# Kernel optimization log

Measured on AMD Instinct MI355X. Metric: run time of the kernel, lower is better.

The kernel has to match this reference:

```python
import jax, jax.numpy as jnp
import numpy as np

B, T, D_IN = 256, 250, 700
H1, H2, D_OUT = 256, 256, 20
B_J0 = 0.01
BETA = 1.8  # adaptation strength (isAdapt=1)
LENS, SCALE, HIGHT, GAMMA = 0.5, 6.0, 0.15, 0.5
SQRT_2PI = float(np.sqrt(2.0 * np.pi))


def _gaussian(x, mu, sigma):
    return jnp.exp(-((x - mu) ** 2) / (2.0 * sigma ** 2)) / (SQRT_2PI * sigma)


@jax.custom_vjp
def act_fun(x):
    # Heaviside spike with multi-Gaussian surrogate gradient (gradient_type='MG')
    return (x > 0).astype(x.dtype)


def _act_fwd(x):
    return act_fun(x), x


def _act_bwd(x, g):
    temp = (_gaussian(x, 0.0, LENS) * (1.0 + HIGHT)
            - _gaussian(x, LENS, SCALE * LENS) * HIGHT
            - _gaussian(x, -LENS, SCALE * LENS) * HIGHT)
    return (g * temp * GAMMA,)


act_fun.defvjp(_act_fwd, _act_bwd)


def setup_inputs() -> dict:
    key = jax.random.key(0)
    ks = jax.random.split(key, 16)
    # binary-ish spike input (SHD spike trains), rand fill
    x = (jax.random.uniform(ks[0], (B, T, D_IN)) < 0.1).astype(jnp.float32)

    def xavier(k, out_d, in_d):
        lim = float(np.sqrt(6.0 / (in_d + out_d)))
        return jax.random.uniform(k, (out_d, in_d), jnp.float32, -lim, lim)

    return {
        "x": x,
        "w_i2h1": xavier(ks[1], H1, D_IN),
        "w_h12h1": xavier(ks[2], H1, H1),
        "w_h12h2": xavier(ks[3], H2, H1),
        "w_h22h2": xavier(ks[4], H2, H2),
        "w_h2o": xavier(ks[5], D_OUT, H2),
        "b_h1": jnp.zeros((H1,), jnp.float32),
        "b_h2": jnp.zeros((H2,), jnp.float32),
        "b_o": jnp.zeros((D_OUT,), jnp.float32),
        "tau_adp_h1": 150.0 + 10.0 * jax.random.normal(ks[6], (H1,), jnp.float32),
        "tau_adp_h2": 150.0 + 10.0 * jax.random.normal(ks[7], (H2,), jnp.float32),
        "tau_m_h1": 20.0 + 5.0 * jax.random.normal(ks[8], (H1,), jnp.float32),
        "tau_m_h2": 20.0 + 5.0 * jax.random.normal(ks[9], (H2,), jnp.float32),
        "tau_m_o": 20.0 + 5.0 * jax.random.normal(ks[10], (D_OUT,), jnp.float32),
    }


def _lif_step(inp, mem, spk, b, alpha, ro):
    # mem_update_adp with params=None, dparams=None, isAdapt=1, dt=1, R_m=1
    b = ro * b + BETA * (1.0 - ro) * spk
    mem = mem * alpha - b * spk + (1.0 - alpha) * inp
    spk = act_fun(mem - b - B_J0)
    return mem, spk, b


def reference(x, w_i2h1, w_h12h1, w_h12h2, w_h22h2, w_h2o,
              b_h1, b_h2, b_o, tau_adp_h1, tau_adp_h2,
              tau_m_h1, tau_m_h2, tau_m_o):
    bsz = x.shape[0]
    h1, h2, d_out = w_i2h1.shape[0], w_h12h2.shape[0], w_h2o.shape[0]

    alpha1 = jnp.exp(-1.0 / tau_m_h1)
    ro1 = jnp.exp(-1.0 / tau_adp_h1)
    alpha2 = jnp.exp(-1.0 / tau_m_h2)
    ro2 = jnp.exp(-1.0 / tau_adp_h2)
    alpha_o = jnp.exp(-1.0 / tau_m_o)

    init = (
        jnp.zeros((bsz, h1)), jnp.zeros((bsz, h1)), jnp.full((bsz, h1), B_J0),
        jnp.zeros((bsz, h2)), jnp.zeros((bsz, h2)), jnp.full((bsz, h2), B_J0),
        jnp.zeros((bsz, d_out)), jnp.zeros((bsz, d_out)),
    )
    xT = jnp.swapaxes(x, 0, 1)  # [T, B, D_in]

    def step(carry, xt):
        mem1, spk1, bb1, mem2, spk2, bb2, mem_o, acc = carry
        h1_in = xt @ w_i2h1.T + spk1 @ w_h12h1.T + b_h1
        mem1, spk1, bb1 = _lif_step(h1_in, mem1, spk1, bb1, alpha1, ro1)
        h2_in = spk1 @ w_h12h2.T + spk2 @ w_h22h2.T + b_h2
        mem2, spk2, bb2 = _lif_step(h2_in, mem2, spk2, bb2, alpha2, ro2)
        o_in = spk2 @ w_h2o.T + b_o
        mem_o = mem_o * alpha_o + (1.0 - alpha_o) * o_in  # output_Neuron
        acc = acc + jax.nn.softmax(mem_o, axis=-1)
        return (mem1, spk1, bb1, mem2, spk2, bb2, mem_o, acc), None

    carry, _ = jax.lax.scan(step, init, xT)
    return carry[-1]  # accumulated softmax over the 250 timesteps, [B, 20]
```

## Files before the change

kernel.cpp:

```cpp
#include <hip/hip_runtime.h>
#include <cstdint>
#include <cstddef>

#define BB 256
#define TT 250
#define DIN 700
#define H1 256
#define H2 256
#define DOUT 20
#define BJ0 0.01f
#define BETAC 1.8f
#define IQSCALE 3.814697265625e-06f

typedef float f32x4 __attribute__((ext_vector_type(4)));
typedef short s16x4 __attribute__((ext_vector_type(4)));
typedef int   i32x4 __attribute__((ext_vector_type(4)));

#define COFF_BL  180224
#define SOFF_T11 180224
#define SOFF_T12 245760
#define SOFF_T22 311296
#define FOFF_W2O 188416
#define FOFF_XP  193536
#define FOFF_MO  16577536
#define N_TRANS  381952

#define BARRIER_LDS() asm volatile("s_waitcnt lgkmcnt(0)\n\ts_barrier" ::: "memory")

__device__ __forceinline__ short q18(float w) {
    float s = w * 262144.0f;
    s = fminf(fmaxf(s, -32767.0f), 32767.0f);
    return (short)__float2int_rn(s);
}

__global__ void transpose_all_k(const float* __restrict__ w_i2h1,
                                const float* __restrict__ w_h12h1,
                                const float* __restrict__ w_h12h2,
                                const float* __restrict__ w_h22h2,
                                const float* __restrict__ w_h2o,
                                signed char* __restrict__ cws,
                                short* __restrict__ sws,
                                float* __restrict__ fws) {
    int i = blockIdx.x * blockDim.x + threadIdx.x;
    if (i < 180224) {
        int h = i / 704, k = i - h * 704;
        int q = (k < DIN) ? (int)q18(w_i2h1[h * DIN + k]) : 0;
        q = q > 32639 ? 32639 : (q < -32640 ? -32640 : q);
        int hi = (q + 128) >> 8;
        int lo = q - (hi << 8);
        cws[i] = (signed char)hi;
        cws[COFF_BL + i] = (signed char)lo;
        return;
    }
    i -= 180224;
    if (i < 65536) { int d = i >> 8, h = i & 255;
        sws[SOFF_T11 + i] = q18(w_h12h1[h * H1 + d]); return; }
    i -= 65536;
    if (i < 65536) { int d = i >> 8, h = i & 255;
        sws[SOFF_T12 + i] = q18(w_h12h2[h * H1 + d]); return; }
    i -= 65536;
    if (i < 65536) { int d = i >> 8, h = i & 255;
        sws[SOFF_T22 + i] = q18(w_h22h2[h * H2 + d]); return; }
    i -= 65536;
    if (i < 5120)  { int j = i / 20, o = i % 20;
        fws[FOFF_W2O + i] = w_h2o[o * H2 + j]; return; }
}

__global__ __launch_bounds__(256) void xgemm_k(const float* __restrict__ x,
                                               const signed char* __restrict__ Bh,
                                               const signed char* __restrict__ Bl,
                                               const float* __restrict__ b_h1,
                                               float* __restrict__ Xp) {
    const int t    = threadIdx.x;
    const int lane = t & 63;
    const int w    = t >> 6;
    const int m0   = blockIdx.x * 32;

    __shared__ __align__(16) signed char Asub[32 * 720];
    __shared__ __align__(16) signed char Bhs[256 * 80];
    __shared__ __align__(16) signed char Bls[256 * 80];

    #pragma unroll
    for (int it = 0; it < 22; ++it) {
        int flat = it * 256 + t;
        int row  = flat / 176;
        int c4   = flat - row * 176;
        unsigned int pk = 0u;
        if (c4 < 175) {
            const float* xr = x + (size_t)(m0 + row) * DIN;
            float4 f = *(const float4*)(xr + (c4 << 2));
            pk = (f.x != 0.f ? 1u : 0u)
               | (f.y != 0.f ? 1u : 0u) << 8
               | (f.z != 0.f ? 1u : 0u) << 16
               | (f.w != 0.f ? 1u : 0u) << 24;
        }
        *(unsigned int*)(Asub + row * 720 + (c4 << 2)) = pk;
    }

    i32x4 acch[2][4], accl[2][4];
    #pragma unroll
    for (int mt = 0; mt < 2; ++mt)
        #pragma unroll
        for (int nt = 0; nt < 4; ++nt) {
            acch[mt][nt] = (i32x4){0, 0, 0, 0};
            accl[mt][nt] = (i32x4){0, 0, 0, 0};
        }

    const int arow  = lane & 15;
    const int kg16  = (lane >> 4) << 4;
    const int bcol0 = w << 6;

    for (int ks = 0; ks < 11; ++ks) {
        __syncthreads();
        #pragma unroll
        for (int it2 = 0; it2 < 4; ++it2) {
            int row = it2 * 64 + (t >> 2);
            int ch  = (t & 3) << 4;
            int go  = row * 704 + ks * 64 + ch;
            *(int4*)(Bhs + row * 80 + ch) = *(const int4*)(Bh + go);
            *(int4*)(Bls + row * 80 + ch) = *(const int4*)(Bl + go);
        }
        __syncthreads();

        const int ko = ks * 64 + kg16;
        i32x4 a0 = *(const i32x4*)(Asub + arow * 720 + ko);
        i32x4 a1 = *(const i32x4*)(Asub + (16 + arow) * 720 + ko);
        #pragma unroll
        for (int nt = 0; nt < 4; ++nt) {
            const int bb = (bcol0 + nt * 16 + arow) * 80 + kg16;
            i32x4 bhf = *(const i32x4*)(Bhs + bb);
            i32x4 blf = *(const i32x4*)(Bls + bb);
            acch[0][nt] = __builtin_amdgcn_mfma_i32_16x16x64_i8(a0, bhf, acch[0][nt], 0, 0, 0);
            acch[1][nt] = __builtin_amdgcn_mfma_i32_16x16x64_i8(a1, bhf, acch[1][nt], 0, 0, 0);
            accl[0][nt] = __builtin_amdgcn_mfma_i32_16x16x64_i8(a0, blf, accl[0][nt], 0, 0, 0);
            accl[1][nt] = __builtin_amdgcn_mfma_i32_16x16x64_i8(a1, blf, accl[1][nt], 0, 0, 0);
        }
    }

    const int crb = (lane >> 4) << 2;
    #pragma unroll
    for (int nt = 0; nt < 4; ++nt) {
        int col = bcol0 + nt * 16 + arow;
        float bias = b_h1[col];
        #pragma unroll
        for (int mt = 0; mt < 2; ++mt) {
            #pragma unroll
            for (int r = 0; r < 4; ++r) {
                int row = m0 + mt * 16 + crb + r;
                int ir = (acch[mt][nt][r] << 8) + accl[mt][nt][r];
                __builtin_nontemporal_store(bias + (float)ir * IQSCALE,
                                            Xp + (size_t)row * H1 + col);
            }
        }
    }
}

__device__ __forceinline__ void add8v(const short* __restrict__ T,
                                      const int* __restrict__ L, int off,
                                      int* a) {
    int4 ea = *(const int4*)(L + off);
    int4 eb = *(const int4*)(L + off + 4);
    s16x4 w0 = *(const s16x4*)(T + ((size_t)ea.x << 8));
    s16x4 w1 = *(const s16x4*)(T + ((size_t)ea.y << 8));
    s16x4 w2 = *(const s16x4*)(T + ((size_t)ea.z << 8));
    s16x4 w3 = *(const s16x4*)(T + ((size_t)ea.w << 8));
    s16x4 w4 = *(const s16x4*)(T + ((size_t)eb.x << 8));
    s16x4 w5 = *(const s16x4*)(T + ((size_t)eb.y << 8));
    s16x4 w6 = *(const s16x4*)(T + ((size_t)eb.z << 8));
    s16x4 w7 = *(const s16x4*)(T + ((size_t)eb.w << 8));
    a[0] += ((w0.x + w1.x) + (w2.x + w3.x)) + ((w4.x + w5.x) + (w6.x + w7.x));
    a[1] += ((w0.y + w1.y) + (w2.y + w3.y)) + ((w4.y + w5.y) + (w6.y + w7.y));
    a[2] += ((w0.z + w1.z) + (w2.z + w3.z)) + ((w4.z + w5.z) + (w6.z + w7.z));
    a[3] += ((w0.w + w1.w) + (w2.w + w3.w)) + ((w4.w + w5.w) + (w6.w + w7.w));
}

__device__ __forceinline__ void tailv(const short* __restrict__ T,
                                      const int* __restrict__ L, int done,
                                      int rem, int* a) {
    if (rem >= 4) {
        int4 e = *(const int4*)(L + done);
        s16x4 w0 = *(const s16x4*)(T + ((size_t)e.x << 8));
        s16x4 w1 = *(const s16x4*)(T + ((size_t)e.y << 8));
        s16x4 w2 = *(const s16x4*)(T + ((size_t)e.z << 8));
        s16x4 w3 = *(const s16x4*)(T + ((size_t)e.w << 8));
        a[0] += (w0.x + w1.x) + (w2.x + w3.x);
        a[1] += (w0.y + w1.y) + (w2.y + w3.y);
        a[2] += (w0.z + w1.z) + (w2.z + w3.z);
        a[3] += (w0.w + w1.w) + (w2.w + w3.w);
        done += 4; rem -= 4;
    }
    if (rem) {
        int4 e = *(const int4*)(L + done);
        s16x4 w0 = *(const s16x4*)(T + ((size_t)e.x << 8));
        a[0] += w0.x; a[1] += w0.y; a[2] += w0.z; a[3] += w0.w;
        if (rem > 1) {
            s16x4 w1 = *(const s16x4*)(T + ((size_t)e.y << 8));
            a[0] += w1.x; a[1] += w1.y; a[2] += w1.z; a[3] += w1.w;
        }
        if (rem > 2) {
            s16x4 w2 = *(const s16x4*)(T + ((size_t)e.z << 8));
            a[0] += w2.x; a[1] += w2.y; a[2] += w2.z; a[3] += w2.w;
        }
    }
}

__device__ __forceinline__ void add8f(const float* __restrict__ T,
                                      const int* __restrict__ L, int off,
                                      float& acc) {
    int4 ea = *(const int4*)(L + off);
    int4 eb = *(const int4*)(L + off + 4);
    acc += T[ea.x * DOUT]; acc += T[ea.y * DOUT];
    acc += T[ea.z * DOUT]; acc += T[ea.w * DOUT];
    acc += T[eb.x * DOUT]; acc += T[eb.y * DOUT];
    acc += T[eb.z * DOUT]; acc += T[eb.w * DOUT];
}

__device__ __forceinline__ void tailf(const float* __restrict__ T,
                                      const int* __restrict__ L, int done,
                                      int rem, float& acc) {
    if (rem >= 4) {
        int4 e = *(const int4*)(L + done);
        acc += T[e.x * DOUT]; acc += T[e.y * DOUT];
        acc += T[e.z * DOUT]; acc += T[e.w * DOUT];
        done += 4; rem -= 4;
    }
    if (rem) {
        int4 e = *(const int4*)(L + done);
        acc += T[e.x * DOUT];
        if (rem > 1) acc += T[e.y * DOUT];
        if (rem > 2) acc += T[e.z * DOUT];
    }
}

__global__ __launch_bounds__(128) void rec_k(
    const float* __restrict__ Xp,
    const short* __restrict__ sT11, const short* __restrict__ sT12,
    const short* __restrict__ sT22, const float* __restrict__ wT2o,
    const float* __restrict__ b_h2, const float* __restrict__ b_o,
    const float* __restrict__ tau_adp_h1, const float* __restrict__ tau_adp_h2,
    const float* __restrict__ tau_m_h1, const float* __restrict__ tau_m_h2,
    const float* __restrict__ tau_m_o,
    float* __restrict__ Mo) {
    const int tid  = threadIdx.x;
    const int lane = tid & 63;
    const int w    = tid >> 6;
    const int c0   = lane << 2;
    const int b    = blockIdx.x;
    const float* __restrict__ XpB = Xp + (size_t)b * TT * H1;
    float* __restrict__ MoB = Mo + (size_t)b * TT * DOUT;

    __shared__ __align__(16) float w2oL[5120];
    __shared__ __align__(16) int lst1s[2][256];
    __shared__ __align__(16) int lst2s[2][256];
    __shared__ int lcnt[2][2];

    for (int k = tid; k < 5120; k += 128) w2oL[k] = wT2o[k];
    for (int k = tid; k < 256; k += 128) {
        lst1s[0][k] = 0; lst1s[1][k] = 0;
        lst2s[0][k] = 0; lst2s[1][k] = 0;
    }
    if (tid < 4) ((int*)lcnt)[tid] = 0;

    float alpha[4], rr[4], inb[4];
    #pragma unroll
    for (int s = 0; s < 4; ++s) {
        if (w == 0) {
            alpha[s] = expf(-1.0f / tau_m_h1[c0 + s]);
            rr[s]    = expf(-1.0f / tau_adp_h1[c0 + s]);
            inb[s]   = 0.f;
        } else {
            alpha[s] = expf(-1.0f / tau_m_h2[c0 + s]);
            rr[s]    = expf(-1.0f / tau_adp_h2[c0 + s]);
            inb[s]   = b_h2[c0 + s];
        }
    }
    float alpo = 0.f, bov = 0.f;
    if (w == 0 && lane < DOUT) { alpo = expf(-1.0f / tau_m_o[lane]); bov = b_o[lane]; }

    float mem[4] = {0.f, 0.f, 0.f, 0.f};
    float bb[4]  = {BJ0, BJ0, BJ0, BJ0};
    float spk[4] = {0.f, 0.f, 0.f, 0.f};
    float memo = 0.f;

    f32x4 xp_cur = (f32x4){0.f, 0.f, 0.f, 0.f};
    if (w == 0) xp_cur = *(const f32x4*)(XpB + c0);
    __syncthreads();

    for (int i = 0; i <= TT + 1; ++i) {
        const int cur = i & 1, nxt = cur ^ 1;

        const int tot1 = lcnt[cur][0];
        const int tot2 = lcnt[cur][1];

        f32x4 xp_nxt = (f32x4){0.f, 0.f, 0.f, 0.f};
        if (w == 0 && i + 1 < TT)
            xp_nxt = *(const f32x4*)(XpB + (size_t)(i + 1) * H1 + c0);

        const int* __restrict__ L1l = lst1s[cur];
        const int* __restrict__ L2l = lst2s[cur];

        int a1[4] = {0, 0, 0, 0};
        int a2[4] = {0, 0, 0, 0};
        float ao = 0.f;

        if (w == 0) {
            if (i < TT) {
                const short* colT = sT11 + c0;
                const int nb8 = tot1 >> 3;
                for (int kk = 0; kk < nb8; ++kk) add8v(colT, L1l, kk << 3, a1);
                tailv(colT, L1l, nb8 << 3, tot1 & 7, a1);
            }
            if (lane < DOUT && i >= 2) {
                const float* colO = w2oL + lane;
                const int nb8 = tot2 >> 3;
                for (int kk = 0; kk < nb8; ++kk) add8f(colO, L2l, kk << 3, ao);
                tailf(colO, L2l, nb8 << 3, tot2 & 7, ao);
            }
        } else if (i >= 1 && i <= TT) {
            const short* cT12 = sT12 + c0;
            const short* cT22 = sT22 + c0;
            const int nb81 = tot1 >> 3;
            const int nb82 = tot2 >> 3;
            const int nbm = nb81 > nb82 ? nb81 : nb82;
            for (int kk = 0; kk < nbm; ++kk) {
                if (kk < nb81) add8v(cT12, L1l, kk << 3, a1);
                if (kk < nb82) add8v(cT22, L2l, kk << 3, a2);
            }
            tailv(cT12, L1l, nb81 << 3, tot1 & 7, a1);
            tailv(cT22, L2l, nb82 << 3, tot2 & 7, a2);
        }

        if (w == 0) {
            int tot = 0;
            if (i < TT) {
                unsigned long long Ms[4];
                #pragma unroll
                for (int s = 0; s < 4; ++s) {
                    float r1 = (float)a1[s] * IQSCALE;
                    bb[s]  = rr[s] * bb[s] + BETAC * (1.f - rr[s]) * spk[s];
                    mem[s] = mem[s] * alpha[s] - bb[s] * spk[s]
                           + (1.f - alpha[s]) * (xp_cur[s] + r1);
                    float ns = (mem[s] - bb[s] - BJ0) > 0.f ? 1.f : 0.f;
                    spk[s] = ns;
                    Ms[s] = __ballot(ns != 0.f ? 1 : 0);
                }
                const unsigned long long below = (1ull << lane) - 1ull;
                int p0 = __popcll(Ms[0]), p1 = __popcll(Ms[1]);
                int p2 = __popcll(Ms[2]), p3 = __popcll(Ms[3]);
                int b1 = p0, b2 = p0 + p1, b3 = p0 + p1 + p2;
                tot = b3 + p3;
                if (spk[0] != 0.f) lst1s[nxt][__popcll(Ms[0] & below)]      = c0;
                if (spk[1] != 0.f) lst1s[nxt][b1 + __popcll(Ms[1] & below)] = c0 + 1;
                if (spk[2] != 0.f) lst1s[nxt][b2 + __popcll(Ms[2] & below)] = c0 + 2;
                if (spk[3] != 0.f) lst1s[nxt][b3 + __popcll(Ms[3] & below)] = c0 + 3;
            }
            if (lane == 0) lcnt[nxt][0] = tot;
            if (lane < DOUT && i >= 2) {
                memo = memo * alpo + (1.f - alpo) * (bov + ao);
                __builtin_nontemporal_store(memo, MoB + (size_t)(i - 2) * DOUT + lane);
            }
        } else {
            int tot = 0;
            if (i >= 1 && i <= TT) {
                unsigned long long Ms[4];
                #pragma unroll
                for (int s = 0; s < 4; ++s) {
                    float r23 = (float)(a1[s] + a2[s]) * IQSCALE;
                    bb[s]  = rr[s] * bb[s] + BETAC * (1.f - rr[s]) * spk[s];
                    mem[s] = mem[s] * alpha[s] - bb[s] * spk[s]
                           + (1.f - alpha[s]) * (inb[s] + r23);
                    float ns = (mem[s] - bb[s] - BJ0) > 0.f ? 1.f : 0.f;
                    spk[s] = ns;
                    Ms[s] = __ballot(ns != 0.f ? 1 : 0);
                }
                const unsigned long long below = (1ull << lane) - 1ull;
                int p0 = __popcll(Ms[0]), p1 = __popcll(Ms[1]);
                int p2 = __popcll(Ms[2]), p3 = __popcll(Ms[3]);
                int b1 = p0, b2 = p0 + p1, b3 = p0 + p1 + p2;
                tot = b3 + p3;
                if (spk[0] != 0.f) lst2s[nxt][__popcll(Ms[0] & below)]      = c0;
                if (spk[1] != 0.f) lst2s[nxt][b1 + __popcll(Ms[1] & below)] = c0 + 1;
                if (spk[2] != 0.f) lst2s[nxt][b2 + __popcll(Ms[2] & below)] = c0 + 2;
                if (spk[3] != 0.f) lst2s[nxt][b3 + __popcll(Ms[3] & below)] = c0 + 3;
            }
            if (lane == 0) lcnt[nxt][1] = tot;
        }

        BARRIER_LDS();
        xp_cur = xp_nxt;
    }
}

__global__ __launch_bounds__(256) void soft_k(const float* __restrict__ Mo,
                                              float* __restrict__ out) {
    const int b = blockIdx.x;
    const int t = threadIdx.x;
    __shared__ float sm[TT][DOUT];

    if (t < TT) {
        const float* row = Mo + ((size_t)b * TT + t) * DOUT;
        float v[DOUT];
        #pragma unroll
        for (int k = 0; k < DOUT; k += 4) {
            float4 r = *(const float4*)(row + k);
            v[k] = r.x; v[k + 1] = r.y; v[k + 2] = r.z; v[k + 3] = r.w;
        }
        float mx = v[0];
        #pragma unroll
        for (int j = 1; j < DOUT; ++j) mx = fmaxf(mx, v[j]);
        float s = 0.f;
        #pragma unroll
        for (int j = 0; j < DOUT; ++j) { v[j] = __expf(v[j] - mx); s += v[j]; }
        float inv = 1.0f / s;
        #pragma unroll
        for (int j = 0; j < DOUT; ++j) sm[t][j] = v[j] * inv;
    }
    __syncthreads();
    if (t < DOUT) {
        float acc = 0.f;
        for (int tt = 0; tt < TT; ++tt) acc += sm[tt][t];
        out[b * DOUT + t] = acc;
    }
}

extern "C" void kernel_launch(void* const* d_in, const int* in_sizes, int n_in,
                              void* d_out, int out_size, void* d_ws, size_t ws_size,
                              hipStream_t stream) {
    const float* x          = (const float*)d_in[0];
    const float* w_i2h1     = (const float*)d_in[1];
    const float* w_h12h1    = (const float*)d_in[2];
    const float* w_h12h2    = (const float*)d_in[3];
    const float* w_h22h2    = (const float*)d_in[4];
    const float* w_h2o      = (const float*)d_in[5];
    const float* b_h1       = (const float*)d_in[6];
    const float* b_h2       = (const float*)d_in[7];
    const float* b_o        = (const float*)d_in[8];
    const float* tau_adp_h1 = (const float*)d_in[9];
    const float* tau_adp_h2 = (const float*)d_in[10];
    const float* tau_m_h1   = (const float*)d_in[11];
    const float* tau_m_h2   = (const float*)d_in[12];
    const float* tau_m_o    = (const float*)d_in[13];

    signed char* cws = (signed char*)d_ws;
    short* sws = (short*)d_ws;
    float* fws = (float*)d_ws;
    const signed char* Bh = cws;
    const signed char* Bl = cws + COFF_BL;
    const short* sT11 = sws + SOFF_T11;
    const short* sT12 = sws + SOFF_T12;
    const short* sT22 = sws + SOFF_T22;
    float* wT2o = fws + FOFF_W2O;
    float* Xp   = fws + FOFF_XP;
    float* Mo   = fws + FOFF_MO;

    transpose_all_k<<<N_TRANS / 256, 256, 0, stream>>>(
        w_i2h1, w_h12h1, w_h12h2, w_h22h2, w_h2o, cws, sws, fws);

    xgemm_k<<<(BB * TT) / 32, 256, 0, stream>>>(x, Bh, Bl, b_h1, Xp);

    rec_k<<<BB, 128, 0, stream>>>(Xp, sT11, sT12, sT22, wT2o,
                                  b_h2, b_o, tau_adp_h1, tau_adp_h2,
                                  tau_m_h1, tau_m_h2, tau_m_o, Mo);

    soft_k<<<BB, 256, 0, stream>>>(Mo, (float*)d_out);
}
```

Measured before the change: 753.5 us.

## Merge two recurrent-layer waves into one wavefront to drop block barriers

```diff
diff --git a/kernel.cpp b/kernel.cpp
--- a/kernel.cpp
+++ b/kernel.cpp
@@ -24,8 +24,6 @@
 #define FOFF_XP  193536
 #define FOFF_MO  16577536
 #define N_TRANS  381952
-
-#define BARRIER_LDS() asm volatile("s_waitcnt lgkmcnt(0)\n\ts_barrier" ::: "memory")
 
 __device__ __forceinline__ short q18(float w) {
     float s = w * 262144.0f;
@@ -232,7 +230,7 @@
     }
 }
 
-__global__ __launch_bounds__(128) void rec_k(
+__global__ __launch_bounds__(64) void rec_k(
     const float* __restrict__ Xp,
     const short* __restrict__ sT11, const short* __restrict__ sT12,
     const short* __restrict__ sT22, const float* __restrict__ wT2o,
@@ -241,9 +239,7 @@
     const float* __restrict__ tau_m_h1, const float* __restrict__ tau_m_h2,
     const float* __restrict__ tau_m_o,
     float* __restrict__ Mo) {
-    const int tid  = threadIdx.x;
-    const int lane = tid & 63;
-    const int w    = tid >> 6;
+    const int lane = threadIdx.x;
     const int c0   = lane << 2;
     const int b    = blockIdx.x;
     const float* __restrict__ XpB = Xp + (size_t)b * TT * H1;
@@ -252,141 +248,134 @@
     __shared__ __align__(16) float w2oL[5120];
     __shared__ __align__(16) int lst1s[2][256];
     __shared__ __align__(16) int lst2s[2][256];
-    __shared__ int lcnt[2][2];
-
-    for (int k = tid; k < 5120; k += 128) w2oL[k] = wT2o[k];
-    for (int k = tid; k < 256; k += 128) {
+
+    for (int k = lane; k < 5120; k += 64) w2oL[k] = wT2o[k];
+    for (int k = lane; k < 256; k += 64) {
         lst1s[0][k] = 0; lst1s[1][k] = 0;
         lst2s[0][k] = 0; lst2s[1][k] = 0;
     }
-    if (tid < 4) ((int*)lcnt)[tid] = 0;
-
-    float alpha[4], rr[4], inb[4];
+
+    float a1c[4], r1c[4], a2c[4], r2c[4], inb[4];
     #pragma unroll
     for (int s = 0; s < 4; ++s) {
-        if (w == 0) {
-            alpha[s] = expf(-1.0f / tau_m_h1[c0 + s]);
-            rr[s]    = expf(-1.0f / tau_adp_h1[c0 + s]);
-            inb[s]   = 0.f;
-        } else {
-            alpha[s] = expf(-1.0f / tau_m_h2[c0 + s]);
-            rr[s]    = expf(-1.0f / tau_adp_h2[c0 + s]);
-            inb[s]   = b_h2[c0 + s];
-        }
+        a1c[s] = expf(-1.0f / tau_m_h1[c0 + s]);
+        r1c[s] = expf(-1.0f / tau_adp_h1[c0 + s]);
+        a2c[s] = expf(-1.0f / tau_m_h2[c0 + s]);
+        r2c[s] = expf(-1.0f / tau_adp_h2[c0 + s]);
+        inb[s] = b_h2[c0 + s];
     }
     float alpo = 0.f, bov = 0.f;
-    if (w == 0 && lane < DOUT) { alpo = expf(-1.0f / tau_m_o[lane]); bov = b_o[lane]; }
-
-    float mem[4] = {0.f, 0.f, 0.f, 0.f};
-    float bb[4]  = {BJ0, BJ0, BJ0, BJ0};
-    float spk[4] = {0.f, 0.f, 0.f, 0.f};
+    if (lane < DOUT) { alpo = expf(-1.0f / tau_m_o[lane]); bov = b_o[lane]; }
+
+    float mem1[4] = {0.f, 0.f, 0.f, 0.f};
+    float bb1[4]  = {BJ0, BJ0, BJ0, BJ0};
+    float spk1[4] = {0.f, 0.f, 0.f, 0.f};
+    float mem2[4] = {0.f, 0.f, 0.f, 0.f};
+    float bb2[4]  = {BJ0, BJ0, BJ0, BJ0};
+    float spk2[4] = {0.f, 0.f, 0.f, 0.f};
     float memo = 0.f;
-
-    f32x4 xp_cur = (f32x4){0.f, 0.f, 0.f, 0.f};
-    if (w == 0) xp_cur = *(const f32x4*)(XpB + c0);
+    int t1c = 0, t2c = 0;
+
+    f32x4 xp_cur = *(const f32x4*)(XpB + c0);
     __syncthreads();
 
     for (int i = 0; i <= TT + 1; ++i) {
         const int cur = i & 1, nxt = cur ^ 1;
 
-        const int tot1 = lcnt[cur][0];
-        const int tot2 = lcnt[cur][1];
-
         f32x4 xp_nxt = (f32x4){0.f, 0.f, 0.f, 0.f};
-        if (w == 0 && i + 1 < TT)
+        if (i + 1 < TT)
             xp_nxt = *(const f32x4*)(XpB + (size_t)(i + 1) * H1 + c0);
 
         const int* __restrict__ L1l = lst1s[cur];
         const int* __restrict__ L2l = lst2s[cur];
-
-        int a1[4] = {0, 0, 0, 0};
-        int a2[4] = {0, 0, 0, 0};
+        const bool d1 = (i < TT);
+        const bool d2 = (i >= 1 && i <= TT);
+        const int nb1 = t1c >> 3, rem1 = t1c & 7;
+        const int nb2 = t2c >> 3, rem2 = t2c & 7;
+
+        int A11[4] = {0, 0, 0, 0};
+        int A12[4] = {0, 0, 0, 0};
+        int A22[4] = {0, 0, 0, 0};
         float ao = 0.f;
 
-        if (w == 0) {
-            if (i < TT) {
-                const short* colT = sT11 + c0;
-                const int nb8 = tot1 >> 3;
-                for (int kk = 0; kk < nb8; ++kk) add8v(colT, L1l, kk << 3, a1);
-                tailv(colT, L1l, nb8 << 3, tot1 & 7, a1);
-            }
-            if (lane < DOUT && i >= 2) {
-                const float* colO = w2oL + lane;
-                const int nb8 = tot2 >> 3;
-                for (int kk = 0; kk < nb8; ++kk) add8f(colO, L2l, kk << 3, ao);
-                tailf(colO, L2l, nb8 << 3, tot2 & 7, ao);
-            }
-        } else if (i >= 1 && i <= TT) {
+        {
+            const short* cT11 = sT11 + c0;
             const short* cT12 = sT12 + c0;
             const short* cT22 = sT22 + c0;
-            const int nb81 = tot1 >> 3;
-            const int nb82 = tot2 >> 3;
-            const int nbm = nb81 > nb82 ? nb81 : nb82;
+            const int nbm = nb1 > nb2 ? nb1 : nb2;
             for (int kk = 0; kk < nbm; ++kk) {
-                if (kk < nb81) add8v(cT12, L1l, kk << 3, a1);
-                if (kk < nb82) add8v(cT22, L2l, kk << 3, a2);
+                if (d1 && kk < nb1) add8v(cT11, L1l, kk << 3, A11);
+                if (d2 && kk < nb1) add8v(cT12, L1l, kk << 3, A12);
+                if (d2 && kk < nb2) add8v(cT22, L2l, kk << 3, A22);
             }
-            tailv(cT12, L1l, nb81 << 3, tot1 & 7, a1);
-            tailv(cT22, L2l, nb82 << 3, tot2 & 7, a2);
-        }
-
-        if (w == 0) {
-            int tot = 0;
-            if (i < TT) {
-                unsigned long long Ms[4];
-                #pragma unroll
-                for (int s = 0; s < 4; ++s) {
-                    float r1 = (float)a1[s] * IQSCALE;
-                    bb[s]  = rr[s] * bb[s] + BETAC * (1.f - rr[s]) * spk[s];
-                    mem[s] = mem[s] * alpha[s] - bb[s] * spk[s]
-                           + (1.f - alpha[s]) * (xp_cur[s] + r1);
-                    float ns = (mem[s] - bb[s] - BJ0) > 0.f ? 1.f : 0.f;
-                    spk[s] = ns;
-                    Ms[s] = __ballot(ns != 0.f ? 1 : 0);
-                }
-                const unsigned long long below = (1ull << lane) - 1ull;
-                int p0 = __popcll(Ms[0]), p1 = __popcll(Ms[1]);
-                int p2 = __popcll(Ms[2]), p3 = __popcll(Ms[3]);
-                int b1 = p0, b2 = p0 + p1, b3 = p0 + p1 + p2;
-                tot = b3 + p3;
-                if (spk[0] != 0.f) lst1s[nxt][__popcll(Ms[0] & below)]      = c0;
-                if (spk[1] != 0.f) lst1s[nxt][b1 + __popcll(Ms[1] & below)] = c0 + 1;
-                if (spk[2] != 0.f) lst1s[nxt][b2 + __popcll(Ms[2] & below)] = c0 + 2;
-                if (spk[3] != 0.f) lst1s[nxt][b3 + __popcll(Ms[3] & below)] = c0 + 3;
+            if (d1) tailv(cT11, L1l, nb1 << 3, rem1, A11);
+            if (d2) {
+                tailv(cT12, L1l, nb1 << 3, rem1, A12);
+                tailv(cT22, L2l, nb2 << 3, rem2, A22);
             }
-            if (lane == 0) lcnt[nxt][0] = tot;
-            if (lane < DOUT && i >= 2) {
-                memo = memo * alpo + (1.f - alpo) * (bov + ao);
-                __builtin_nontemporal_store(memo, MoB + (size_t)(i - 2) * DOUT + lane);
+        }
+        if (lane < DOUT && i >= 2) {
+            const float* colO = w2oL + lane;
+            for (int kk = 0; kk < nb2; ++kk) add8f(colO, L2l, kk << 3, ao);
+            tailf(colO, L2l, nb2 << 3, rem2, ao);
+        }
+
+        const unsigned long long below = (1ull << lane) - 1ull;
+
+        if (d1) {
+            unsigned long long Ms[4];
+            #pragma unroll
+            for (int s = 0; s < 4; ++s) {
+                float r1 = (float)A11[s] * IQSCALE;
+                bb1[s]  = r1c[s] * bb1[s] + BETAC * (1.f - r1c[s]) * spk1[s];
+                mem1[s] = mem1[s] * a1c[s] - bb1[s] * spk1[s]
+                        + (1.f - a1c[s]) * (xp_cur[s] + r1);
+                float ns = (mem1[s] - bb1[s] - BJ0) > 0.f ? 1.f : 0.f;
+                spk1[s] = ns;
+                Ms[s] = __ballot(ns != 0.f ? 1 : 0);
             }
+            int p0 = __popcll(Ms[0]), p1 = __popcll(Ms[1]);
+            int p2 = __popcll(Ms[2]), p3 = __popcll(Ms[3]);
+            int o1 = p0, o2 = p0 + p1, o3 = p0 + p1 + p2;
+            if (spk1[0] != 0.f) lst1s[nxt][__popcll(Ms[0] & below)]      = c0;
+            if (spk1[1] != 0.f) lst1s[nxt][o1 + __popcll(Ms[1] & below)] = c0 + 1;
+            if (spk1[2] != 0.f) lst1s[nxt][o2 + __popcll(Ms[2] & below)] = c0 + 2;
+            if (spk1[3] != 0.f) lst1s[nxt][o3 + __popcll(Ms[3] & below)] = c0 + 3;
+            t1c = o3 + p3;
         } else {
-            int tot = 0;
-            if (i >= 1 && i <= TT) {
-                unsigned long long Ms[4];
-                #pragma unroll
-                for (int s = 0; s < 4; ++s) {
-                    float r23 = (float)(a1[s] + a2[s]) * IQSCALE;
-                    bb[s]  = rr[s] * bb[s] + BETAC * (1.f - rr[s]) * spk[s];
-                    mem[s] = mem[s] * alpha[s] - bb[s] * spk[s]
-                           + (1.f - alpha[s]) * (inb[s] + r23);
-                    float ns = (mem[s] - bb[s] - BJ0) > 0.f ? 1.f : 0.f;
-                    spk[s] = ns;
-                    Ms[s] = __ballot(ns != 0.f ? 1 : 0);
-                }
-                const unsigned long long below = (1ull << lane) - 1ull;
-                int p0 = __popcll(Ms[0]), p1 = __popcll(Ms[1]);
-                int p2 = __popcll(Ms[2]), p3 = __popcll(Ms[3]);
-                int b1 = p0, b2 = p0 + p1, b3 = p0 + p1 + p2;
-                tot = b3 + p3;
-                if (spk[0] != 0.f) lst2s[nxt][__popcll(Ms[0] & below)]      = c0;
-                if (spk[1] != 0.f) lst2s[nxt][b1 + __popcll(Ms[1] & below)] = c0 + 1;
-                if (spk[2] != 0.f) lst2s[nxt][b2 + __popcll(Ms[2] & below)] = c0 + 2;
-                if (spk[3] != 0.f) lst2s[nxt][b3 + __popcll(Ms[3] & below)] = c0 + 3;
+            t1c = 0;
+        }
+
+        if (d2) {
+            unsigned long long Ms[4];
+            #pragma unroll
+            for (int s = 0; s < 4; ++s) {
+                float r23 = (float)(A12[s] + A22[s]) * IQSCALE;
+                bb2[s]  = r2c[s] * bb2[s] + BETAC * (1.f - r2c[s]) * spk2[s];
+                mem2[s] = mem2[s] * a2c[s] - bb2[s] * spk2[s]
+                        + (1.f - a2c[s]) * (inb[s] + r23);
+                float ns = (mem2[s] - bb2[s] - BJ0) > 0.f ? 1.f : 0.f;
+                spk2[s] = ns;
+                Ms[s] = __ballot(ns != 0.f ? 1 : 0);
             }
-            if (lane == 0) lcnt[nxt][1] = tot;
-        }
-
-        BARRIER_LDS();
+            int p0 = __popcll(Ms[0]), p1 = __popcll(Ms[1]);
+            int p2 = __popcll(Ms[2]), p3 = __popcll(Ms[3]);
+            int o1 = p0, o2 = p0 + p1, o3 = p0 + p1 + p2;
+            if (spk2[0] != 0.f) lst2s[nxt][__popcll(Ms[0] & below)]      = c0;
+            if (spk2[1] != 0.f) lst2s[nxt][o1 + __popcll(Ms[1] & below)] = c0 + 1;
+            if (spk2[2] != 0.f) lst2s[nxt][o2 + __popcll(Ms[2] & below)] = c0 + 2;
+            if (spk2[3] != 0.f) lst2s[nxt][o3 + __popcll(Ms[3] & below)] = c0 + 3;
+            t2c = o3 + p3;
+        } else {
+            t2c = 0;
+        }
+
+        if (lane < DOUT && i >= 2) {
+            memo = memo * alpo + (1.f - alpo) * (bov + ao);
+            __builtin_nontemporal_store(memo, MoB + (size_t)(i - 2) * DOUT + lane);
+        }
+
+        asm volatile("s_waitcnt lgkmcnt(0)" ::: "memory");
         xp_cur = xp_nxt;
     }
 }
@@ -458,9 +447,9 @@
 
     xgemm_k<<<(BB * TT) / 32, 256, 0, stream>>>(x, Bh, Bl, b_h1, Xp);
 
-    rec_k<<<BB, 128, 0, stream>>>(Xp, sT11, sT12, sT22, wT2o,
-                                  b_h2, b_o, tau_adp_h1, tau_adp_h2,
-                                  tau_m_h1, tau_m_h2, tau_m_o, Mo);
+    rec_k<<<BB, 64, 0, stream>>>(Xp, sT11, sT12, sT22, wT2o,
+                                 b_h2, b_o, tau_adp_h1, tau_adp_h2,
+                                 tau_m_h1, tau_m_h2, tau_m_o, Mo);
 
     soft_k<<<BB, 256, 0, stream>>>(Mo, (float*)d_out);
 }
```

Measured after the change: 979.2 us. +30.0%, slower.
